# Kernel tuning notes

Measured on AMD Instinct MI355X. Metric: run time of the kernel, lower is better.

Reference implementation:

```python
import jax, jax.numpy as jnp
import numpy as np

BN_EPS = 1e-5


def setup_inputs() -> dict:
    key = jax.random.key(0)
    ks = jax.random.split(key, 4)
    N, C, T, V, S = 64, 64, 300, 25, 3
    x = jax.random.normal(ks[0], (N, C, T, V), dtype=jnp.float32)
    PA = jax.random.uniform(ks[1], (S, V, V), dtype=jnp.float32)
    # 1x1 conv weights per subset, branch-init scale sqrt(2/(out*1*1*branches))
    Wc = jax.random.normal(ks[2], (S, C, C), dtype=jnp.float32) * np.sqrt(2.0 / (C * S))
    bc = jnp.zeros((S, C), dtype=jnp.float32)
    gamma = jnp.ones((C,), dtype=jnp.float32)
    beta = jnp.zeros((C,), dtype=jnp.float32)
    return {"x": x, "PA": PA, "Wc": Wc, "bc": bc, "gamma": gamma, "beta": beta}


def reference(x, PA, Wc, bc, gamma, beta):
    # x: [N,C,T,V]; PA: [S,V,V]; Wc: [S,Cout,Cin]; bc: [S,Cout]
    # L2_norm: per-column L2 norm along dim=1 of each subset adjacency
    A = PA / (jnp.linalg.norm(PA, axis=1, keepdims=True) + 1e-4)  # [S,V,V]
    # For each subset: (x.view(N,CT,V) @ A[s]) then 1x1 conv, summed over subsets.
    # out[n,o,t,w] = sum_s sum_c sum_v x[n,c,t,v] * A[s,v,w] * Wc[s,o,c] + sum_s bc[s,o]
    y = jnp.einsum('nctv,svw,soc->notw', x, A, Wc)
    y = y + bc.sum(axis=0)[None, :, None, None]
    # BatchNorm2d (training-mode batch statistics) over (N,T,V) per channel
    mean = y.mean(axis=(0, 2, 3), keepdims=True)
    var = y.var(axis=(0, 2, 3), keepdims=True)
    y = (y - mean) * jax.lax.rsqrt(var + BN_EPS)
    y = y * gamma[None, :, None, None] + beta[None, :, None, None]
    # residual (identity since in_channels == out_channels) + ReLU
    return jax.nn.relu(y + x)
```

## Files before the change

kernel.cpp:

```cpp
#include <hip/hip_runtime.h>
#include <hip/hip_bf16.h>
#include <math.h>

typedef __attribute__((ext_vector_type(8))) short short8v;
typedef __attribute__((ext_vector_type(4))) float f32x4;

#define NB 64
#define CC 64
#define TT 300
#define VV 25
#define SS 3
#define TB 4
#define TBLK (TT/TB)
#define TILES (NB*TBLK)
#define TOTAL4 (NB*CC*TT*VV/4)
#define PERC4  (TT*VV/4)
#define CNTF   480000.0f

#define AFA_BYTES 36864
#define WCF_BYTES 49152
#define YOFF_BYTES 131072

static __device__ __forceinline__ unsigned short f2bf(float f){
    union { __hip_bfloat16 h; unsigned short s; } u;
    u.h = __float2bfloat16(f);
    return u.s;
}
static __device__ __forceinline__ float bf2f(unsigned short b){
    return __uint_as_float(((unsigned)b) << 16);
}
static __device__ __forceinline__ void pack2(const f32x4& z, unsigned& d0, unsigned& d1){
    d0 = (unsigned)f2bf(z[0]) | ((unsigned)f2bf(z[1]) << 16);
    d1 = (unsigned)f2bf(z[2]) | ((unsigned)f2bf(z[3]) << 16);
}
static __device__ __forceinline__ short8v mk8(unsigned q0,unsigned q1,unsigned q2,unsigned q3){
    union { unsigned u[4]; short8v v; } x;
    x.u[0]=q0; x.u[1]=q1; x.u[2]=q2; x.u[3]=q3;
    return x.v;
}

__global__ void gcn_prep(const float* __restrict__ PA, const float* __restrict__ Wc,
                         float* __restrict__ ws)
{
    __shared__ float inv[SS][VV];
    const int tid = threadIdx.x;
    const int nz = 8192 / 8;
    for (int i = tid; i < nz; i += 384) ws[blockIdx.x * nz + i] = 0.f;
    if (blockIdx.x != 0) return;

    if (tid < SS*VV){
        int s = tid/VV, w = tid%VV;
        float sum = 0.f;
        for (int v=0; v<VV; ++v){ float p = PA[s*VV*VV + v*VV + w]; sum = fmaf(p,p,sum); }
        inv[s][w] = 1.f/(sqrtf(sum)+1e-4f);
    }
    __syncthreads();
    {
        int s = tid/128, rem = tid%128, nt = rem/64, lane = rem%64;
        int w = nt*16 + (lane&15), g = lane>>4;
        short8v vals;
        #pragma unroll
        for (int j=0;j<8;++j){
            int v = 8*g + j;
            float f = (v<VV && w<VV) ? PA[s*VV*VV + v*VV + w]*inv[s][w] : 0.f;
            vals[j] = (short)f2bf(f);
        }
        *(short8v*)((char*)ws + AFA_BYTES + (size_t)((s*2+nt)*64 + lane)*16) = vals;
    }
    for (int fid = tid; fid < SS*4*2*64; fid += 384){
        int lane = fid & 63;
        int kt = (fid >> 6) & 1;
        int ot = (fid >> 7) & 3;
        int s  = fid >> 9;
        int o  = 16*ot + (lane & 15);
        int c0 = kt*32 + 8*(lane >> 4);
        short8v vals;
        #pragma unroll
        for (int j=0;j<8;++j) vals[j] = (short)f2bf(Wc[((size_t)s*CC + o)*CC + c0 + j]);
        *(short8v*)((char*)ws + WCF_BYTES + (size_t)fid*16) = vals;
    }
}

template<bool YB>
__global__ __launch_bounds__(256,4) void gcn_main_kernel(
    const float* __restrict__ x, float* __restrict__ ws,
    float* __restrict__ yf32, __hip_bfloat16* __restrict__ ybf)
{
    __shared__ __align__(16) unsigned short lds[CC*100];

    const int tid  = threadIdx.x;
    const int lane = tid & 63;
    const int wv   = tid >> 6;
    const int l15  = lane & 15, g = lane >> 4;
    const int n    = blockIdx.x / TBLK;
    const int t0   = (blockIdx.x % TBLK) * TB;
    const int t    = t0 + wv;

    short8v axf[4];
    #pragma unroll
    for (int mt=0; mt<4; ++mt){
        const int c = 16*mt + l15;
        const float* p = x + ((size_t)(n*CC + c)*TT + t)*VV + 8*g;
        short8v f;
        if (g < 3){
            float4 a = *(const float4*)p;
            float4 b = *(const float4*)(p+4);
            f[0]=(short)f2bf(a.x); f[1]=(short)f2bf(a.y); f[2]=(short)f2bf(a.z); f[3]=(short)f2bf(a.w);
            f[4]=(short)f2bf(b.x); f[5]=(short)f2bf(b.y); f[6]=(short)f2bf(b.z); f[7]=(short)f2bf(b.w);
        } else {
            f[0]=(short)f2bf(p[0]);
            f[1]=0; f[2]=0; f[3]=0; f[4]=0; f[5]=0; f[6]=0; f[7]=0;
        }
        axf[mt] = f;
    }

    const short8v* afrag = (const short8v*)((const char*)ws + AFA_BYTES);
    const short8v* wfrag = (const short8v*)((const char*)ws + WCF_BYTES);

    const f32x4 zf = {0.f,0.f,0.f,0.f};
    f32x4 yacc[4][2];
    #pragma unroll
    for (int ot=0; ot<4; ++ot){ yacc[ot][0]=zf; yacc[ot][1]=zf; }

    const int sLo = 32*(g&1) + l15;
    const int sHi = sLo + 16;
    const bool hi = (lane >= 32);

    #pragma unroll
    for (int s=0; s<SS; ++s){
        short8v aA0 = afrag[(s*2+0)*64 + lane];
        short8v aA1 = afrag[(s*2+1)*64 + lane];
        #pragma unroll
        for (int kt=0; kt<2; ++kt){
            f32x4 z00 = __builtin_amdgcn_mfma_f32_16x16x32_bf16(axf[2*kt+0], aA0, zf, 0,0,0);
            f32x4 z01 = __builtin_amdgcn_mfma_f32_16x16x32_bf16(axf[2*kt+0], aA1, zf, 0,0,0);
            f32x4 z10 = __builtin_amdgcn_mfma_f32_16x16x32_bf16(axf[2*kt+1], aA0, zf, 0,0,0);
            f32x4 z11 = __builtin_amdgcn_mfma_f32_16x16x32_bf16(axf[2*kt+1], aA1, zf, 0,0,0);
            unsigned pLo0n0, pLo1n0, pLo0n1, pLo1n1;
            unsigned pHi0n0, pHi1n0, pHi0n1, pHi1n1;
            pack2(z00, pLo0n0, pLo1n0);
            pack2(z01, pLo0n1, pLo1n1);
            pack2(z10, pHi0n0, pHi1n0);
            pack2(z11, pHi0n1, pHi1n1);
            unsigned a0,b0,a1,b1,a2,b2,a3,b3;
            a0=__shfl(pLo0n0,sLo); b0=__shfl(pHi0n0,sLo);
            a1=__shfl(pLo1n0,sLo); b1=__shfl(pHi1n0,sLo);
            a2=__shfl(pLo0n0,sHi); b2=__shfl(pHi0n0,sHi);
            a3=__shfl(pLo1n0,sHi); b3=__shfl(pHi1n0,sHi);
            short8v bz0 = mk8(hi?b0:a0, hi?b1:a1, hi?b2:a2, hi?b3:a3);
            a0=__shfl(pLo0n1,sLo); b0=__shfl(pHi0n1,sLo);
            a1=__shfl(pLo1n1,sLo); b1=__shfl(pHi1n1,sLo);
            a2=__shfl(pLo0n1,sHi); b2=__shfl(pHi0n1,sHi);
            a3=__shfl(pLo1n1,sHi); b3=__shfl(pHi1n1,sHi);
            short8v bz1 = mk8(hi?b0:a0, hi?b1:a1, hi?b2:a2, hi?b3:a3);
            #pragma unroll
            for (int ot=0; ot<4; ++ot){
                short8v wc = wfrag[((s*4+ot)*2+kt)*64 + lane];
                yacc[ot][0] = __builtin_amdgcn_mfma_f32_16x16x32_bf16(wc, bz0, yacc[ot][0], 0,0,0);
                yacc[ot][1] = __builtin_amdgcn_mfma_f32_16x16x32_bf16(wc, bz1, yacc[ot][1], 0,0,0);
            }
        }
    }

    #pragma unroll
    for (int ot=0; ot<4; ++ot){
        #pragma unroll
        for (int r=0; r<4; ++r){
            const int o = 16*ot + 4*g + r;
            lds[o*100 + wv*25 + l15] = f2bf(yacc[ot][0][r]);
            if (l15 < VV-16)
                lds[o*100 + wv*25 + 16 + l15] = f2bf(yacc[ot][1][r]);
        }
    }
    __syncthreads();

    for (int i = tid; i < 1600; i += 256){
        const int row = i / 25;
        const int c8  = i % 25;
        uint2 d = *(const uint2*)&lds[row*100 + c8*4];
        const size_t base = (size_t)(n*CC + row)*(TT*VV) + (size_t)t0*VV + c8*4;
        if (YB){
            *(uint2*)((unsigned short*)ybf + base) = d;
        } else {
            float4 f;
            f.x = bf2f((unsigned short)(d.x & 0xffff));
            f.y = bf2f((unsigned short)(d.x >> 16));
            f.z = bf2f((unsigned short)(d.y & 0xffff));
            f.w = bf2f((unsigned short)(d.y >> 16));
            *(float4*)(yf32 + base) = f;
        }
    }

    {
        const int o = tid >> 2, q = tid & 3;
        float s1 = 0.f, s2 = 0.f;
        for (int gr = q; gr < 25; gr += 4){
            uint2 d = *(const uint2*)&lds[o*100 + gr*4];
            float a0 = bf2f((unsigned short)(d.x & 0xffff));
            float a1 = bf2f((unsigned short)(d.x >> 16));
            float a2 = bf2f((unsigned short)(d.y & 0xffff));
            float a3 = bf2f((unsigned short)(d.y >> 16));
            s1 += (a0+a1)+(a2+a3);
            s2 = fmaf(a0,a0,fmaf(a1,a1,fmaf(a2,a2,fmaf(a3,a3,s2))));
        }
        s1 += __shfl_xor(s1,1); s1 += __shfl_xor(s1,2);
        s2 += __shfl_xor(s2,1); s2 += __shfl_xor(s2,2);
        if (q == 0){
            atomicAdd(&ws[n*128 + o],      s1);
            atomicAdd(&ws[n*128 + 64 + o], s2);
        }
    }
}

__global__ void gcn_finalize_kernel(const float* __restrict__ gamma,
                                    const float* __restrict__ beta,
                                    float* __restrict__ ws)
{
    const int o = threadIdx.x;
    if (o < CC) {
        float s = 0.f, q = 0.f;
        for (int n = 0; n < NB; ++n){
            s += ws[n*128 + o];
            q += ws[n*128 + 64 + o];
        }
        const float mean = s / CNTF;
        const float var  = q / CNTF - mean * mean;
        const float sc   = gamma[o] * rsqrtf(var + 1e-5f);
        ws[8192 + o] = sc;
        ws[8256 + o] = beta[o] - mean * sc;
    }
}

template<bool YB>
__global__ __launch_bounds__(256) void gcn_bn_relu_kernel(
    const float* __restrict__ x, float* __restrict__ out,
    const float* __restrict__ ws, const unsigned short* __restrict__ ybf)
{
    for (int i = blockIdx.x * 256 + threadIdx.x; i < TOTAL4; i += gridDim.x * 256) {
        const int c = (i / PERC4) & (CC - 1);
        const float sc = ws[8192 + c];
        const float sh = ws[8256 + c];
        float4 yv;
        if (YB){
            uint2 yb = *(const uint2*)&ybf[4*i];
            yv.x = bf2f((unsigned short)(yb.x & 0xffff));
            yv.y = bf2f((unsigned short)(yb.x >> 16));
            yv.z = bf2f((unsigned short)(yb.y & 0xffff));
            yv.w = bf2f((unsigned short)(yb.y >> 16));
        } else {
            yv = reinterpret_cast<float4*>(out)[i];
        }
        float4 xv = reinterpret_cast<const float4*>(x)[i];
        float4 r;
        r.x = fmaxf(fmaf(yv.x, sc, sh) + xv.x, 0.f);
        r.y = fmaxf(fmaf(yv.y, sc, sh) + xv.y, 0.f);
        r.z = fmaxf(fmaf(yv.z, sc, sh) + xv.z, 0.f);
        r.w = fmaxf(fmaf(yv.w, sc, sh) + xv.w, 0.f);
        reinterpret_cast<float4*>(out)[i] = r;
    }
}

extern "C" void kernel_launch(void* const* d_in, const int* in_sizes, int n_in,
                              void* d_out, int out_size, void* d_ws, size_t ws_size,
                              hipStream_t stream)
{
    const float* x     = (const float*)d_in[0];
    const float* PA    = (const float*)d_in[1];
    const float* Wc    = (const float*)d_in[2];
    const float* gamma = (const float*)d_in[4];
    const float* beta  = (const float*)d_in[5];
    float* out = (float*)d_out;
    float* ws  = (float*)d_ws;

    const size_t ybytes = (size_t)NB*CC*TT*VV*2;
    const bool yb = ws_size >= (size_t)YOFF_BYTES + ybytes;
    __hip_bfloat16* ybf = (__hip_bfloat16*)((char*)d_ws + YOFF_BYTES);

    gcn_prep<<<8, 384, 0, stream>>>(PA, Wc, ws);
    if (yb){
        gcn_main_kernel<true><<<TILES, 256, 0, stream>>>(x, ws, out, ybf);
        gcn_finalize_kernel<<<1, 64, 0, stream>>>(gamma, beta, ws);
        gcn_bn_relu_kernel<true><<<4096, 256, 0, stream>>>(x, out, ws, (const unsigned short*)ybf);
    } else {
        gcn_main_kernel<false><<<TILES, 256, 0, stream>>>(x, ws, out, ybf);
        gcn_finalize_kernel<<<1, 64, 0, stream>>>(gamma, beta, ws);
        gcn_bn_relu_kernel<false><<<4096, 256, 0, stream>>>(x, out, ws, (const unsigned short*)ybf);
    }
}
```

Measured before the change: 132.7 us.

## Switch GCN matmuls to 32x32x16 MFMA with permlane32 swap relayout

Replaces the 16x16x32 bf16 MFMA tiling with 32x32x16 MFMA for both the adjacency product and the 1x1 conv. Fragment layouts for A and Wc are regenerated in the prep kernel to match. The intermediate relayout between the two matmuls now uses permlane32_swap, falling back to xor shuffles, instead of many __shfl calls. This is meant to cut instruction count and cross-lane traffic, at the cost of padding V=25 up to 32 columns (more wasted MFMA work) and a non-unrolled subset loop.

```diff
diff --git a/kernel.cpp b/kernel.cpp
--- a/kernel.cpp
+++ b/kernel.cpp
@@ -4,6 +4,8 @@
 
 typedef __attribute__((ext_vector_type(8))) short short8v;
 typedef __attribute__((ext_vector_type(4))) float f32x4;
+typedef __attribute__((ext_vector_type(16))) float f32x16;
+typedef __attribute__((ext_vector_type(2))) unsigned uint2v;
 
 #define NB 64
 #define CC 64
@@ -29,15 +31,24 @@
 static __device__ __forceinline__ float bf2f(unsigned short b){
     return __uint_as_float(((unsigned)b) << 16);
 }
-static __device__ __forceinline__ void pack2(const f32x4& z, unsigned& d0, unsigned& d1){
-    d0 = (unsigned)f2bf(z[0]) | ((unsigned)f2bf(z[1]) << 16);
-    d1 = (unsigned)f2bf(z[2]) | ((unsigned)f2bf(z[3]) << 16);
+static __device__ __forceinline__ void packq(float z0, float z1, float z2, float z3,
+                                             unsigned& d0, unsigned& d1){
+    d0 = (unsigned)f2bf(z0) | ((unsigned)f2bf(z1) << 16);
+    d1 = (unsigned)f2bf(z2) | ((unsigned)f2bf(z3) << 16);
 }
 static __device__ __forceinline__ short8v mk8(unsigned q0,unsigned q1,unsigned q2,unsigned q3){
     union { unsigned u[4]; short8v v; } x;
     x.u[0]=q0; x.u[1]=q1; x.u[2]=q2; x.u[3]=q3;
     return x.v;
 }
+
+#if __has_builtin(__builtin_amdgcn_permlane32_swap)
+#define SWAP32(a,b,ra,rb) { uint2v _r = __builtin_amdgcn_permlane32_swap((a),(b),false,false); (ra)=_r[0]; (rb)=_r[1]; }
+#else
+#define SWAP32(a,b,ra,rb) { unsigned _sa=(unsigned)__shfl_xor((int)(a),32); \
+                            unsigned _sb=(unsigned)__shfl_xor((int)(b),32); \
+                            (ra) = hi ? _sb : (a); (rb) = hi ? (b) : _sa; }
+#endif
 
 __global__ void gcn_prep(const float* __restrict__ PA, const float* __restrict__ Wc,
                          float* __restrict__ ws)
@@ -56,28 +67,30 @@
     }
     __syncthreads();
     {
-        int s = tid/128, rem = tid%128, nt = rem/64, lane = rem%64;
-        int w = nt*16 + (lane&15), g = lane>>4;
+        int fid = tid >> 6, lane = tid & 63;
+        int s = fid >> 1, ksv = fid & 1;
+        int w = lane & 31, h = lane >> 5;
+        int v0 = 16*ksv + 8*h;
         short8v vals;
         #pragma unroll
         for (int j=0;j<8;++j){
-            int v = 8*g + j;
+            int v = v0 + j;
             float f = (v<VV && w<VV) ? PA[s*VV*VV + v*VV + w]*inv[s][w] : 0.f;
             vals[j] = (short)f2bf(f);
         }
-        *(short8v*)((char*)ws + AFA_BYTES + (size_t)((s*2+nt)*64 + lane)*16) = vals;
-    }
-    for (int fid = tid; fid < SS*4*2*64; fid += 384){
-        int lane = fid & 63;
-        int kt = (fid >> 6) & 1;
-        int ot = (fid >> 7) & 3;
-        int s  = fid >> 9;
-        int o  = 16*ot + (lane & 15);
-        int c0 = kt*32 + 8*(lane >> 4);
+        *(short8v*)((char*)ws + AFA_BYTES + (size_t)(fid*64 + lane)*16) = vals;
+    }
+    for (int fid4 = tid; fid4 < SS*2*4*64; fid4 += 384){
+        int lane = fid4 & 63;
+        int ks = (fid4 >> 6) & 3;
+        int ot = (fid4 >> 8) & 1;
+        int s  = fid4 >> 9;
+        int o  = 32*ot + (lane & 31);
+        int c0 = 16*ks + 8*(lane >> 5);
         short8v vals;
         #pragma unroll
         for (int j=0;j<8;++j) vals[j] = (short)f2bf(Wc[((size_t)s*CC + o)*CC + c0 + j]);
-        *(short8v*)((char*)ws + WCF_BYTES + (size_t)fid*16) = vals;
+        *(short8v*)((char*)ws + WCF_BYTES + (size_t)fid4*16) = vals;
     }
 }
 
@@ -91,85 +104,84 @@
     const int tid  = threadIdx.x;
     const int lane = tid & 63;
     const int wv   = tid >> 6;
-    const int l15  = lane & 15, g = lane >> 4;
+    const int l31  = lane & 31, h = lane >> 5;
+    const bool hi  = (lane >= 32);
+    (void)hi;
     const int n    = blockIdx.x / TBLK;
     const int t0   = (blockIdx.x % TBLK) * TB;
     const int t    = t0 + wv;
 
-    short8v axf[4];
+    short8v axf[2][2];
     #pragma unroll
-    for (int mt=0; mt<4; ++mt){
-        const int c = 16*mt + l15;
-        const float* p = x + ((size_t)(n*CC + c)*TT + t)*VV + 8*g;
-        short8v f;
-        if (g < 3){
-            float4 a = *(const float4*)p;
-            float4 b = *(const float4*)(p+4);
-            f[0]=(short)f2bf(a.x); f[1]=(short)f2bf(a.y); f[2]=(short)f2bf(a.z); f[3]=(short)f2bf(a.w);
-            f[4]=(short)f2bf(b.x); f[5]=(short)f2bf(b.y); f[6]=(short)f2bf(b.z); f[7]=(short)f2bf(b.w);
-        } else {
-            f[0]=(short)f2bf(p[0]);
-            f[1]=0; f[2]=0; f[3]=0; f[4]=0; f[5]=0; f[6]=0; f[7]=0;
-        }
-        axf[mt] = f;
+    for (int mt=0; mt<2; ++mt){
+        #pragma unroll
+        for (int ksv=0; ksv<2; ++ksv){
+            const int c  = 32*mt + l31;
+            const int v0 = 16*ksv + 8*h;
+            const float* p = x + ((size_t)(n*CC + c)*TT + t)*VV + v0;
+            short8v f;
+            if (v0 < 24){
+                float4 a = *(const float4*)p;
+                float4 b = *(const float4*)(p+4);
+                f[0]=(short)f2bf(a.x); f[1]=(short)f2bf(a.y); f[2]=(short)f2bf(a.z); f[3]=(short)f2bf(a.w);
+                f[4]=(short)f2bf(b.x); f[5]=(short)f2bf(b.y); f[6]=(short)f2bf(b.z); f[7]=(short)f2bf(b.w);
+            } else {
+                f[0]=(short)f2bf(p[0]);
+                f[1]=0; f[2]=0; f[3]=0; f[4]=0; f[5]=0; f[6]=0; f[7]=0;
+            }
+            axf[mt][ksv] = f;
+        }
     }
 
     const short8v* afrag = (const short8v*)((const char*)ws + AFA_BYTES);
     const short8v* wfrag = (const short8v*)((const char*)ws + WCF_BYTES);
 
-    const f32x4 zf = {0.f,0.f,0.f,0.f};
-    f32x4 yacc[4][2];
+    f32x16 zf16;
     #pragma unroll
-    for (int ot=0; ot<4; ++ot){ yacc[ot][0]=zf; yacc[ot][1]=zf; }
-
-    const int sLo = 32*(g&1) + l15;
-    const int sHi = sLo + 16;
-    const bool hi = (lane >= 32);
-
-    #pragma unroll
+    for (int i=0;i<16;++i) zf16[i] = 0.f;
+    f32x16 yacc[2];
+    yacc[0] = zf16; yacc[1] = zf16;
+
+    #pragma unroll 1
     for (int s=0; s<SS; ++s){
         short8v aA0 = afrag[(s*2+0)*64 + lane];
         short8v aA1 = afrag[(s*2+1)*64 + lane];
-        #pragma unroll
-        for (int kt=0; kt<2; ++kt){
-            f32x4 z00 = __builtin_amdgcn_mfma_f32_16x16x32_bf16(axf[2*kt+0], aA0, zf, 0,0,0);
-            f32x4 z01 = __builtin_amdgcn_mfma_f32_16x16x32_bf16(axf[2*kt+0], aA1, zf, 0,0,0);
-            f32x4 z10 = __builtin_amdgcn_mfma_f32_16x16x32_bf16(axf[2*kt+1], aA0, zf, 0,0,0);
-            f32x4 z11 = __builtin_amdgcn_mfma_f32_16x16x32_bf16(axf[2*kt+1], aA1, zf, 0,0,0);
-            unsigned pLo0n0, pLo1n0, pLo0n1, pLo1n1;
-            unsigned pHi0n0, pHi1n0, pHi0n1, pHi1n1;
-            pack2(z00, pLo0n0, pLo1n0);
-            pack2(z01, pLo0n1, pLo1n1);
-            pack2(z10, pHi0n0, pHi1n0);
-            pack2(z11, pHi0n1, pHi1n1);
-            unsigned a0,b0,a1,b1,a2,b2,a3,b3;
-            a0=__shfl(pLo0n0,sLo); b0=__shfl(pHi0n0,sLo);
-            a1=__shfl(pLo1n0,sLo); b1=__shfl(pHi1n0,sLo);
-            a2=__shfl(pLo0n0,sHi); b2=__shfl(pHi0n0,sHi);
-            a3=__shfl(pLo1n0,sHi); b3=__shfl(pHi1n0,sHi);
-            short8v bz0 = mk8(hi?b0:a0, hi?b1:a1, hi?b2:a2, hi?b3:a3);
-            a0=__shfl(pLo0n1,sLo); b0=__shfl(pHi0n1,sLo);
-            a1=__shfl(pLo1n1,sLo); b1=__shfl(pHi1n1,sLo);
-            a2=__shfl(pLo0n1,sHi); b2=__shfl(pHi0n1,sHi);
-            a3=__shfl(pLo1n1,sHi); b3=__shfl(pHi1n1,sHi);
-            short8v bz1 = mk8(hi?b0:a0, hi?b1:a1, hi?b2:a2, hi?b3:a3);
+
+        unsigned pk[2][4][2];
+        #pragma unroll
+        for (int mt=0; mt<2; ++mt){
+            f32x16 z = __builtin_amdgcn_mfma_f32_32x32x16_bf16(axf[mt][0], aA0, zf16, 0,0,0);
+            z = __builtin_amdgcn_mfma_f32_32x32x16_bf16(axf[mt][1], aA1, z, 0,0,0);
             #pragma unroll
-            for (int ot=0; ot<4; ++ot){
-                short8v wc = wfrag[((s*4+ot)*2+kt)*64 + lane];
-                yacc[ot][0] = __builtin_amdgcn_mfma_f32_16x16x32_bf16(wc, bz0, yacc[ot][0], 0,0,0);
-                yacc[ot][1] = __builtin_amdgcn_mfma_f32_16x16x32_bf16(wc, bz1, yacc[ot][1], 0,0,0);
+            for (int q=0; q<4; ++q)
+                packq(z[4*q], z[4*q+1], z[4*q+2], z[4*q+3], pk[mt][q][0], pk[mt][q][1]);
+        }
+
+        #pragma unroll
+        for (int mt=0; mt<2; ++mt){
+            #pragma unroll
+            for (int ksl=0; ksl<2; ++ksl){
+                const int ks = 2*mt + ksl;
+                unsigned r0d0, r1d0, r0d1, r1d1;
+                SWAP32(pk[mt][2*ksl][0],   pk[mt][2*ksl+1][0], r0d0, r1d0);
+                SWAP32(pk[mt][2*ksl][1],   pk[mt][2*ksl+1][1], r0d1, r1d1);
+                short8v bz = mk8(r0d0, r0d1, r1d0, r1d1);
+                #pragma unroll
+                for (int ot=0; ot<2; ++ot){
+                    short8v wc = wfrag[((s*2+ot)*4+ks)*64 + lane];
+                    yacc[ot] = __builtin_amdgcn_mfma_f32_32x32x16_bf16(wc, bz, yacc[ot], 0,0,0);
+                }
             }
         }
     }
 
     #pragma unroll
-    for (int ot=0; ot<4; ++ot){
-        #pragma unroll
-        for (int r=0; r<4; ++r){
-            const int o = 16*ot + 4*g + r;
-            lds[o*100 + wv*25 + l15] = f2bf(yacc[ot][0][r]);
-            if (l15 < VV-16)
-                lds[o*100 + wv*25 + 16 + l15] = f2bf(yacc[ot][1][r]);
+    for (int ot=0; ot<2; ++ot){
+        #pragma unroll
+        for (int r=0; r<16; ++r){
+            const int o = 32*ot + (r&3) + 8*(r>>2) + 4*h;
+            if (l31 < VV)
+                lds[o*100 + wv*25 + l31] = f2bf(yacc[ot][r]);
         }
     }
     __syncthreads();
```

Measured after the change: 121.8 us. -8.2%, faster.
